# Kernel optimization log

Hardware: AMD Instinct MI355X
Metric: run time of the kernel (lower is better)

## Reference

```python
import jax, jax.numpy as jnp
import numpy as np

N_EXPERTS = 8
D_MODEL = 1024
D_FF = 4096
N_TOKENS = 2048
TOP_K = 2


def _init_expert_weight(key, shape):
    # torch init: bound = sqrt(3) * (sqrt(1/3) / sqrt(fan_in)) = 1/sqrt(fan_in), fan_in = shape[1]
    bound = 1.0 / np.sqrt(shape[1])
    return jax.random.uniform(key, shape, jnp.float32, -bound, bound)


def setup_inputs() -> dict:
    key = jax.random.key(0)
    kx, ki, kw, k1, k2, k3 = jax.random.split(key, 6)
    x = jax.random.normal(kx, (N_TOKENS, D_MODEL), jnp.float32)
    expert_indices = jax.random.randint(ki, (N_TOKENS, TOP_K), 0, N_EXPERTS, jnp.int32)
    expert_weights = jax.random.uniform(kw, (N_TOKENS, TOP_K), jnp.float32)
    w1 = _init_expert_weight(k1, (N_EXPERTS, D_MODEL, D_FF))
    w2 = _init_expert_weight(k2, (N_EXPERTS, D_MODEL, D_FF))
    w3 = _init_expert_weight(k3, (N_EXPERTS, D_FF, D_MODEL))
    return {"x": x, "expert_indices": expert_indices, "expert_weights": expert_weights,
            "w1": w1, "w2": w2, "w3": w3}


def reference(x, expert_indices, expert_weights, w1, w2, w3):
    n_tokens, d_model = x.shape
    top_k = expert_indices.shape[1]
    n_experts = w1.shape[0]
    A = n_tokens * top_k  # total assignments; static capacity per expert (no overflow possible)

    flat_e = expert_indices.reshape(-1)            # [A]
    flat_w = expert_weights.reshape(-1)            # [A]
    tok_idx = jnp.repeat(jnp.arange(n_tokens), top_k)  # [A]

    order = jnp.argsort(flat_e, stable=True)
    s_tok = tok_idx[order]
    s_e = flat_e[order]
    s_w = flat_w[order]

    counts = jnp.bincount(flat_e, length=n_experts)            # [E]
    seg_starts = jnp.concatenate([jnp.zeros((1,), counts.dtype), jnp.cumsum(counts)[:-1]])
    pos = jnp.arange(A) - seg_starts[s_e]                       # position within expert segment

    # dispatch: padded per-expert batch [E, A, d]
    padded = jnp.zeros((n_experts, A, d_model), x.dtype).at[s_e, pos].set(x[s_tok])

    gate = jax.nn.silu(jnp.einsum('ecd,edf->ecf', padded, w1))
    value = jnp.einsum('ecd,edf->ecf', padded, w2)
    hidden = gate * value
    expert_out = jnp.einsum('ecf,efd->ecd', hidden, w3)        # [E, A, d]

    # combine: gather per-assignment outputs, weight, scatter-add back to tokens
    y = expert_out[s_e, pos] * s_w[:, None]                    # [A, d]
    out = jnp.zeros((n_tokens, d_model), x.dtype).at[s_tok].add(y)
    return out
```

## Files before the change

kernel.cpp:

```cpp
#include <hip/hip_runtime.h>
#include <stdint.h>

#define N_EXPERTS 8
#define D_MODEL 1024
#define D_FF 4096
#define N_TOKENS 2048
#define ASSN 4096
#define ROWS 4352
#define BK 64

using bfrag = __attribute__((ext_vector_type(8))) short;
using f32x4 = __attribute__((ext_vector_type(4))) float;
typedef unsigned short u16;

__device__ __forceinline__ u16 f2bf(float f) {
  uint32_t u = __builtin_bit_cast(uint32_t, f);
  u += 0x7fffu + ((u >> 16) & 1u);
  return (u16)(u >> 16);
}

__device__ __forceinline__ void gll16(const void* g, void* l) {
  __builtin_amdgcn_global_load_lds(
      (const __attribute__((address_space(1))) void*)g,
      (__attribute__((address_space(3))) void*)l, 16, 0, 0);
}

__global__ void k_setup(const int* __restrict__ eidx, const float* __restrict__ ew,
                        int* __restrict__ rowmap, int* __restrict__ arow,
                        int* __restrict__ counts, int* __restrict__ offs) {
  __shared__ int sc[N_EXPERTS], so[N_EXPERTS];
  int t = threadIdx.x;
  if (t < N_EXPERTS) sc[t] = 0;
  __syncthreads();
  for (int a = t; a < ASSN; a += 256) atomicAdd(&sc[eidx[a]], 1);
  __syncthreads();
  if (t == 0) {
    int run = 0;
    for (int e = 0; e < N_EXPERTS; e++) {
      counts[e] = sc[e]; offs[e] = run; so[e] = run; run += sc[e];
    }
  }
  __syncthreads();
  for (int a = t; a < ASSN; a += 256) {
    int e = eidx[a];
    int p = atomicAdd(&so[e], 1);
    rowmap[p] = a;
    arow[a] = p;
  }
}

__global__ void k_gather(const float* __restrict__ x, const int* __restrict__ rowmap,
                         u16* __restrict__ Xg) {
  int r = blockIdx.x, t = threadIdx.x;
  uint2 o;
  if (r < ASSN) {
    int tok = rowmap[r] >> 1;
    float4 v = *(const float4*)(x + (size_t)tok * D_MODEL + t * 4);
    o.x = (uint32_t)f2bf(v.x) | ((uint32_t)f2bf(v.y) << 16);
    o.y = (uint32_t)f2bf(v.z) | ((uint32_t)f2bf(v.w) << 16);
  } else {
    o.x = 0u; o.y = 0u;
  }
  *(uint2*)(Xg + (size_t)r * D_MODEL + t * 4) = o;
}

__global__ void k_convt(const float* __restrict__ src, u16* __restrict__ dst,
                        int K, int N) {
  const int e = blockIdx.z;
  src += (size_t)e * K * N;
  dst += (size_t)e * K * N;
  const int n0 = blockIdx.x << 6;
  const int kbase = blockIdx.y << 9;
  __shared__ uint32_t T2[64 * 33];
  const int t = threadIdx.x;
  const int i4 = (t & 15) << 2;
  const int q  = t >> 4;
  const int n = t >> 2, seg = t & 3;
  for (int it = 0; it < 8; ++it) {
    const int k0 = kbase + (it << 6);
    if (it) __syncthreads();
    #pragma unroll
    for (int p = 0; p < 2; p++) {
      const int kp = q + (p << 4);
      const float4 r0 = *(const float4*)(src + (size_t)(k0 + 2 * kp    ) * N + n0 + i4);
      const float4 r1 = *(const float4*)(src + (size_t)(k0 + 2 * kp + 1) * N + n0 + i4);
      T2[(i4 + 0) * 33 + kp] = (uint32_t)f2bf(r0.x) | ((uint32_t)f2bf(r1.x) << 16);
      T2[(i4 + 1) * 33 + kp] = (uint32_t)f2bf(r0.y) | ((uint32_t)f2bf(r1.y) << 16);
      T2[(i4 + 2) * 33 + kp] = (uint32_t)f2bf(r0.z) | ((uint32_t)f2bf(r1.z) << 16);
      T2[(i4 + 3) * 33 + kp] = (uint32_t)f2bf(r0.w) | ((uint32_t)f2bf(r1.w) << 16);
    }
    __syncthreads();
    uint32_t w[8];
    #pragma unroll
    for (int j = 0; j < 8; j++) w[j] = T2[n * 33 + (seg << 3) + j];
    u16* d = dst + (size_t)(n0 + n) * K + k0 + (seg << 4);
    *(uint4*)d = *(uint4*)&w[0];
    *(uint4*)(d + 8) = *(uint4*)&w[4];
  }
}

__launch_bounds__(512, 2)
__global__ void k_gemm1(const u16* __restrict__ Xg,
                        const u16* __restrict__ w1t, const u16* __restrict__ w2t,
                        const int* __restrict__ counts, const int* __restrict__ offs,
                        u16* __restrict__ H) {
  const int e = blockIdx.z, nt = blockIdx.x, mt = blockIdx.y;
  const int cnt = counts[e];
  if (mt * 256 >= cnt) return;
  const int row0 = offs[e] + mt * 256;
  const int mrem = cnt - mt * 256;
  const int n0 = nt * 128;

  __shared__ u16 As[2][256 * BK];
  __shared__ u16 B1s[2][128 * BK];
  __shared__ u16 B2s[2][128 * BK];

  const int tid = threadIdx.x;
  const int lane = tid & 63, wave = tid >> 6;
  const int l16 = lane & 15, quad = lane >> 4;
  const int wm = (wave >> 1) << 6;
  const int wn = (wave & 1) << 6;

  const int swz = ((lane & 7) ^ ((lane >> 3) & 7)) << 3;
  const int arow = wave * 32 + (lane >> 3);
  const int brow = wave * 16 + (lane >> 3);

  const u16* pA  = Xg + (size_t)(row0 + arow) * D_MODEL + swz;
  const size_t ebase = (size_t)e * D_MODEL * D_FF;
  const u16* pB1 = w1t + ebase + (size_t)(n0 + brow) * D_MODEL + swz;
  const u16* pB2 = w2t + ebase + (size_t)(n0 + brow) * D_MODEL + swz;

  const int sA = l16 & 7;
  const int slot0 = ((quad    ) ^ sA) << 3;
  const int slot1 = ((quad + 4) ^ sA) << 3;

  f32x4 acc1[4][4] = {};
  f32x4 acc2[4][4] = {};

#define STAGE1(buf)                                                  \
  do {                                                               \
    gll16(pA,                &As[buf][(wave * 32     ) * BK]);       \
    gll16(pA +  8 * D_MODEL, &As[buf][(wave * 32 +  8) * BK]);       \
    gll16(pA + 16 * D_MODEL, &As[buf][(wave * 32 + 16) * BK]);       \
    gll16(pA + 24 * D_MODEL, &As[buf][(wave * 32 + 24) * BK]);       \
    gll16(pB1,               &B1s[buf][(wave * 16    ) * BK]);       \
    gll16(pB1 + 8 * D_MODEL, &B1s[buf][(wave * 16 + 8) * BK]);       \
    gll16(pB2,               &B2s[buf][(wave * 16    ) * BK]);       \
    gll16(pB2 + 8 * D_MODEL, &B2s[buf][(wave * 16 + 8) * BK]);       \
    pA += BK; pB1 += BK; pB2 += BK;                                  \
  } while (0)

  STAGE1(0);
  for (int t = 0; t < 16; ++t) {
    const int c = t & 1;
    if (t < 15) {
      STAGE1(1 - c);
      asm volatile("s_waitcnt vmcnt(8)" ::: "memory");
    } else {
      asm volatile("s_waitcnt vmcnt(0)" ::: "memory");
    }
    __builtin_amdgcn_sched_barrier(0);
    __builtin_amdgcn_s_barrier();
    __builtin_amdgcn_sched_barrier(0);

    bfrag a0[4], b10[4], b20[4];
    #pragma unroll
    for (int i = 0; i < 4; i++)
      a0[i] = *(const bfrag*)&As[c][(wm + i * 16 + l16) * BK + slot0];
    #pragma unroll
    for (int j = 0; j < 4; j++) {
      b10[j] = *(const bfrag*)&B1s[c][(wn + j * 16 + l16) * BK + slot0];
      b20[j] = *(const bfrag*)&B2s[c][(wn + j * 16 + l16) * BK + slot0];
    }
    asm volatile("s_waitcnt lgkmcnt(0)" ::: "memory");
    __builtin_amdgcn_sched_barrier(0);
    __builtin_amdgcn_s_setprio(1);
    #pragma unroll
    for (int i = 0; i < 4; i++) {
      #pragma unroll
      for (int j = 0; j < 4; j++) {
        acc1[i][j] = __builtin_amdgcn_mfma_f32_16x16x32_bf16(a0[i], b10[j], acc1[i][j], 0, 0, 0);
        acc2[i][j] = __builtin_amdgcn_mfma_f32_16x16x32_bf16(a0[i], b20[j], acc2[i][j], 0, 0, 0);
      }
    }
    __builtin_amdgcn_s_setprio(0);

    bfrag a1[4], b11[4], b21[4];
    #pragma unroll
    for (int i = 0; i < 4; i++)
      a1[i] = *(const bfrag*)&As[c][(wm + i * 16 + l16) * BK + slot1];
    #pragma unroll
    for (int j = 0; j < 4; j++) {
      b11[j] = *(const bfrag*)&B1s[c][(wn + j * 16 + l16) * BK + slot1];
      b21[j] = *(const bfrag*)&B2s[c][(wn + j * 16 + l16) * BK + slot1];
    }
    asm volatile("s_waitcnt lgkmcnt(0)" ::: "memory");
    __builtin_amdgcn_sched_barrier(0);
    __builtin_amdgcn_s_setprio(1);
    #pragma unroll
    for (int i = 0; i < 4; i++) {
      #pragma unroll
      for (int j = 0; j < 4; j++) {
        acc1[i][j] = __builtin_amdgcn_mfma_f32_16x16x32_bf16(a1[i], b11[j], acc1[i][j], 0, 0, 0);
        acc2[i][j] = __builtin_amdgcn_mfma_f32_16x16x32_bf16(a1[i], b21[j], acc2[i][j], 0, 0, 0);
      }
    }
    __builtin_amdgcn_s_setprio(0);

    __builtin_amdgcn_sched_barrier(0);
    __builtin_amdgcn_s_barrier();
    __builtin_amdgcn_sched_barrier(0);
  }
#undef STAGE1

  #pragma unroll
  for (int i = 0; i < 4; i++) {
    #pragma unroll
    for (int p = 0; p < 4; p++) {
      const int mloc = wm + i * 16 + quad * 4 + p;
      if (mloc < mrem) {
        u16* dst = H + (size_t)(row0 + mloc) * D_FF + n0 + wn + l16;
        #pragma unroll
        for (int j = 0; j < 4; j++) {
          float g = acc1[i][j][p];
          float vv = acc2[i][j][p];
          float h = g / (1.0f + __expf(-g)) * vv;
          dst[j * 16] = f2bf(h);
        }
      }
    }
  }
}

__launch_bounds__(512, 2)
__global__ void k_gemm2(const u16* __restrict__ H, const u16* __restrict__ w3t,
                        const int* __restrict__ counts, const int* __restrict__ offs,
                        float* __restrict__ Y0, float* __restrict__ Y1) {
  const int e = blockIdx.z >> 1, khalf = blockIdx.z & 1;
  const int nt = blockIdx.x, mt = blockIdx.y;
  const int cnt = counts[e];
  if (mt * 256 >= cnt) return;
  const int row0 = offs[e] + mt * 256;
  const int mrem = cnt - mt * 256;
  const int n0 = nt * 128;
  float* __restrict__ Y = khalf ? Y1 : Y0;

  __shared__ u16 As[2][256 * BK];
  __shared__ u16 Bs[2][128 * BK];

  const int tid = threadIdx.x;
  const int lane = tid & 63, wave = tid >> 6;
  const int l16 = lane & 15, quad = lane >> 4;
  const int wm = (wave >> 1) << 6;
  const int wn = (wave & 1) << 6;

  const int swz = ((lane & 7) ^ ((lane >> 3) & 7)) << 3;
  const int arow = wave * 32 + (lane >> 3);
  const int brow = wave * 16 + (lane >> 3);

  const u16* pA = H + (size_t)(row0 + arow) * D_FF + khalf * 2048 + swz;
  const u16* pB = w3t + (size_t)e * D_FF * D_MODEL
                + (size_t)(n0 + brow) * D_FF + khalf * 2048 + swz;

  const int sA = l16 & 7;
  const int slot0 = ((quad    ) ^ sA) << 3;
  const int slot1 = ((quad + 4) ^ sA) << 3;

  f32x4 acc[4][4] = {};

#define STAGE2(buf)                                                  \
  do {                                                               \
    gll16(pA,               &As[buf][(wave * 32     ) * BK]);        \
    gll16(pA +  8 * D_FF,   &As[buf][(wave * 32 +  8) * BK]);        \
    gll16(pA + 16 * D_FF,   &As[buf][(wave * 32 + 16) * BK]);        \
    gll16(pA + 24 * D_FF,   &As[buf][(wave * 32 + 24) * BK]);        \
    gll16(pB,               &Bs[buf][(wave * 16    ) * BK]);         \
    gll16(pB + 8 * D_FF,    &Bs[buf][(wave * 16 + 8) * BK]);         \
    pA += BK; pB += BK;                                              \
  } while (0)

  STAGE2(0);
  for (int t = 0; t < 32; ++t) {
    const int c = t & 1;
    if (t < 31) {
      STAGE2(1 - c);
      asm volatile("s_waitcnt vmcnt(6)" ::: "memory");
    } else {
      asm volatile("s_waitcnt vmcnt(0)" ::: "memory");
    }
    __builtin_amdgcn_sched_barrier(0);
    __builtin_amdgcn_s_barrier();
    __builtin_amdgcn_sched_barrier(0);

    bfrag a0[4], b0[4];
    #pragma unroll
    for (int i = 0; i < 4; i++)
      a0[i] = *(const bfrag*)&As[c][(wm + i * 16 + l16) * BK + slot0];
    #pragma unroll
    for (int j = 0; j < 4; j++)
      b0[j] = *(const bfrag*)&Bs[c][(wn + j * 16 + l16) * BK + slot0];
    asm volatile("s_waitcnt lgkmcnt(0)" ::: "memory");
    __builtin_amdgcn_sched_barrier(0);
    __builtin_amdgcn_s_setprio(1);
    #pragma unroll
    for (int i = 0; i < 4; i++) {
      #pragma unroll
      for (int j = 0; j < 4; j++)
        acc[i][j] = __builtin_amdgcn_mfma_f32_16x16x32_bf16(a0[i], b0[j], acc[i][j], 0, 0, 0);
    }
    __builtin_amdgcn_s_setprio(0);

    bfrag a1[4], b1[4];
    #pragma unroll
    for (int i = 0; i < 4; i++)
      a1[i] = *(const bfrag*)&As[c][(wm + i * 16 + l16) * BK + slot1];
    #pragma unroll
    for (int j = 0; j < 4; j++)
      b1[j] = *(const bfrag*)&Bs[c][(wn + j * 16 + l16) * BK + slot1];
    asm volatile("s_waitcnt lgkmcnt(0)" ::: "memory");
    __builtin_amdgcn_sched_barrier(0);
    __builtin_amdgcn_s_setprio(1);
    #pragma unroll
    for (int i = 0; i < 4; i++) {
      #pragma unroll
      for (int j = 0; j < 4; j++)
        acc[i][j] = __builtin_amdgcn_mfma_f32_16x16x32_bf16(a1[i], b1[j], acc[i][j], 0, 0, 0);
    }
    __builtin_amdgcn_s_setprio(0);

    __builtin_amdgcn_sched_barrier(0);
    __builtin_amdgcn_s_barrier();
    __builtin_amdgcn_sched_barrier(0);
  }
#undef STAGE2

  #pragma unroll
  for (int i = 0; i < 4; i++) {
    #pragma unroll
    for (int p = 0; p < 4; p++) {
      const int mloc = wm + i * 16 + quad * 4 + p;
      if (mloc < mrem) {
        float* dst = Y + (size_t)(row0 + mloc) * D_MODEL + n0 + wn + l16;
        #pragma unroll
        for (int j = 0; j < 4; j++) dst[j * 16] = acc[i][j][p];
      }
    }
  }
}

__global__ void k_combine(const float* __restrict__ Y0, const float* __restrict__ Y1,
                          const int* __restrict__ arow, const float* __restrict__ ew,
                          float* __restrict__ out) {
  const int tk = blockIdx.x;
  const int d = threadIdx.x * 4;
  const int a0 = tk * 2, a1 = tk * 2 + 1;
  const int r0 = arow[a0], r1 = arow[a1];
  const float w0 = ew[a0], w1 = ew[a1];
  const float4 p0 = *(const float4*)(Y0 + (size_t)r0 * D_MODEL + d);
  const float4 q0 = *(const float4*)(Y1 + (size_t)r0 * D_MODEL + d);
  const float4 p1 = *(const float4*)(Y0 + (size_t)r1 * D_MODEL + d);
  const float4 q1 = *(const float4*)(Y1 + (size_t)r1 * D_MODEL + d);
  float4 r;
  r.x = w0 * (p0.x + q0.x) + w1 * (p1.x + q1.x);
  r.y = w0 * (p0.y + q0.y) + w1 * (p1.y + q1.y);
  r.z = w0 * (p0.z + q0.z) + w1 * (p1.z + q1.z);
  r.w = w0 * (p0.w + q0.w) + w1 * (p1.w + q1.w);
  *(float4*)(out + (size_t)tk * D_MODEL + d) = r;
}

extern "C" void kernel_launch(void* const* d_in, const int* in_sizes, int n_in,
                              void* d_out, int out_size, void* d_ws, size_t ws_size,
                              hipStream_t stream) {
  const float* x  = (const float*)d_in[0];
  const int* eidx = (const int*)d_in[1];
  const float* ew = (const float*)d_in[2];
  const float* w1 = (const float*)d_in[3];
  const float* w2 = (const float*)d_in[4];
  const float* w3 = (const float*)d_in[5];
  float* out = (float*)d_out;

  char* ws = (char*)d_ws;
  int*   rowmap = (int*)(ws);
  int*   arow   = (int*)(ws + 16384);
  int*   counts = (int*)(ws + 32768);
  int*   offs   = (int*)(ws + 32768 + 64);
  const size_t D0 = 65536;
  const size_t SZ_XG = (size_t)ROWS * D_MODEL * 2;
  const size_t SZ_HB = (size_t)ROWS * D_FF * 2;
  const size_t SZ_Y  = (size_t)ROWS * D_MODEL * 4;
  const size_t SZ_W  = (size_t)N_EXPERTS * D_MODEL * D_FF * 2;
  u16*   Xg  = (u16*)(ws + D0);
  u16*   Hb  = (u16*)(ws + D0 + SZ_XG);
  float* Y0  = (float*)(ws + D0 + SZ_XG + SZ_HB);
  float* Y1  = (float*)(ws + D0 + SZ_XG + SZ_HB + SZ_Y);
  u16*   wt1 = (u16*)(ws + D0 + SZ_XG + SZ_HB + 2 * SZ_Y);
  u16*   wt2 = wt1 + SZ_W / 2;
  u16*   wt3 = wt1;

  k_setup<<<1, 256, 0, stream>>>(eidx, ew, rowmap, arow, counts, offs);
  k_gather<<<ROWS, 256, 0, stream>>>(x, rowmap, Xg);
  k_convt<<<dim3(D_FF / 64, 2, N_EXPERTS), 256, 0, stream>>>(w1, wt1, D_MODEL, D_FF);
  k_convt<<<dim3(D_FF / 64, 2, N_EXPERTS), 256, 0, stream>>>(w2, wt2, D_MODEL, D_FF);
  k_gemm1<<<dim3(D_FF / 128, 16, N_EXPERTS), 512, 0, stream>>>(Xg, wt1, wt2, counts, offs, Hb);
  k_convt<<<dim3(D_MODEL / 64, 8, N_EXPERTS), 256, 0, stream>>>(w3, wt3, D_FF, D_MODEL);
  k_gemm2<<<dim3(D_MODEL / 128, 16, N_EXPERTS * 2), 512, 0, stream>>>(Hb, wt3, counts, offs, Y0, Y1);
  k_combine<<<N_TOKENS, 256, 0, stream>>>(Y0, Y1, arow, ew, out);
}
```

Before: 659.9 us.

## Interleave prefetch with split MFMA phases and flatten weight-transpose grid

The GEMM main loops are restructured into several barrier-separated phases: global-to-LDS prefetches for the next tile are spread across the MFMA phases instead of issued all at once, and B fragments are loaded one matrix at a time to cut register pressure. A full vmcnt(0) wait now sits at the end of each iteration, in place of the partial wait at the start. The weight conversion/transpose kernel is changed so each block handles a single 64x64 tile, giving many more blocks for better occupancy. The extra barriers add synchronization overhead in exchange for finer overlap of loads and compute.

New measurement: 678.5 us. +2.8%, slower.

```diff
diff --git a/kernel.cpp b/kernel.cpp
--- a/kernel.cpp
+++ b/kernel.cpp
@@ -24,6 +24,12 @@
       (const __attribute__((address_space(1))) void*)g,
       (__attribute__((address_space(3))) void*)l, 16, 0, 0);
 }
+
+#define LGKM0_SB()  do { asm volatile("s_waitcnt lgkmcnt(0)" ::: "memory"); \
+                         __builtin_amdgcn_sched_barrier(0); } while (0)
+#define BAR_SB()    do { __builtin_amdgcn_sched_barrier(0); \
+                         __builtin_amdgcn_s_barrier(); \
+                         __builtin_amdgcn_sched_barrier(0); } while (0)
 
 __global__ void k_setup(const int* __restrict__ eidx, const float* __restrict__ ew,
                         int* __restrict__ rowmap, int* __restrict__ arow,
@@ -66,37 +72,34 @@
 
 __global__ void k_convt(const float* __restrict__ src, u16* __restrict__ dst,
                         int K, int N) {
-  const int e = blockIdx.z;
+  const int e = blockIdx.y;
   src += (size_t)e * K * N;
   dst += (size_t)e * K * N;
-  const int n0 = blockIdx.x << 6;
-  const int kbase = blockIdx.y << 9;
+  const int ntn = N >> 6;
+  const int n0 = (blockIdx.x % ntn) << 6;
+  const int k0 = (blockIdx.x / ntn) << 6;
   __shared__ uint32_t T2[64 * 33];
   const int t = threadIdx.x;
   const int i4 = (t & 15) << 2;
   const int q  = t >> 4;
+  #pragma unroll
+  for (int p = 0; p < 2; p++) {
+    const int kp = q + (p << 4);
+    const float4 r0 = *(const float4*)(src + (size_t)(k0 + 2 * kp    ) * N + n0 + i4);
+    const float4 r1 = *(const float4*)(src + (size_t)(k0 + 2 * kp + 1) * N + n0 + i4);
+    T2[(i4 + 0) * 33 + kp] = (uint32_t)f2bf(r0.x) | ((uint32_t)f2bf(r1.x) << 16);
+    T2[(i4 + 1) * 33 + kp] = (uint32_t)f2bf(r0.y) | ((uint32_t)f2bf(r1.y) << 16);
+    T2[(i4 + 2) * 33 + kp] = (uint32_t)f2bf(r0.z) | ((uint32_t)f2bf(r1.z) << 16);
+    T2[(i4 + 3) * 33 + kp] = (uint32_t)f2bf(r0.w) | ((uint32_t)f2bf(r1.w) << 16);
+  }
+  __syncthreads();
   const int n = t >> 2, seg = t & 3;
-  for (int it = 0; it < 8; ++it) {
-    const int k0 = kbase + (it << 6);
-    if (it) __syncthreads();
-    #pragma unroll
-    for (int p = 0; p < 2; p++) {
-      const int kp = q + (p << 4);
-      const float4 r0 = *(const float4*)(src + (size_t)(k0 + 2 * kp    ) * N + n0 + i4);
-      const float4 r1 = *(const float4*)(src + (size_t)(k0 + 2 * kp + 1) * N + n0 + i4);
-      T2[(i4 + 0) * 33 + kp] = (uint32_t)f2bf(r0.x) | ((uint32_t)f2bf(r1.x) << 16);
-      T2[(i4 + 1) * 33 + kp] = (uint32_t)f2bf(r0.y) | ((uint32_t)f2bf(r1.y) << 16);
-      T2[(i4 + 2) * 33 + kp] = (uint32_t)f2bf(r0.z) | ((uint32_t)f2bf(r1.z) << 16);
-      T2[(i4 + 3) * 33 + kp] = (uint32_t)f2bf(r0.w) | ((uint32_t)f2bf(r1.w) << 16);
-    }
-    __syncthreads();
-    uint32_t w[8];
-    #pragma unroll
-    for (int j = 0; j < 8; j++) w[j] = T2[n * 33 + (seg << 3) + j];
-    u16* d = dst + (size_t)(n0 + n) * K + k0 + (seg << 4);
-    *(uint4*)d = *(uint4*)&w[0];
-    *(uint4*)(d + 8) = *(uint4*)&w[4];
-  }
+  uint32_t w[8];
+  #pragma unroll
+  for (int j = 0; j < 8; j++) w[j] = T2[n * 33 + (seg << 3) + j];
+  u16* d = dst + (size_t)(n0 + n) * K + k0 + (seg << 4);
+  *(uint4*)d = *(uint4*)&w[0];
+  *(uint4*)(d + 8) = *(uint4*)&w[4];
 }
 
 __launch_bounds__(512, 2)
@@ -122,13 +125,13 @@
   const int wn = (wave & 1) << 6;
 
   const int swz = ((lane & 7) ^ ((lane >> 3) & 7)) << 3;
-  const int arow = wave * 32 + (lane >> 3);
-  const int brow = wave * 16 + (lane >> 3);
-
-  const u16* pA  = Xg + (size_t)(row0 + arow) * D_MODEL + swz;
+  const int arw = wave * 32 + (lane >> 3);
+  const int brw = wave * 16 + (lane >> 3);
+
+  const u16* pA  = Xg + (size_t)(row0 + arw) * D_MODEL + swz;
   const size_t ebase = (size_t)e * D_MODEL * D_FF;
-  const u16* pB1 = w1t + ebase + (size_t)(n0 + brow) * D_MODEL + swz;
-  const u16* pB2 = w2t + ebase + (size_t)(n0 + brow) * D_MODEL + swz;
+  const u16* pB1 = w1t + ebase + (size_t)(n0 + brw) * D_MODEL + swz;
+  const u16* pB2 = w2t + ebase + (size_t)(n0 + brw) * D_MODEL + swz;
 
   const int sA = l16 & 7;
   const int slot0 = ((quad    ) ^ sA) << 3;
@@ -137,81 +140,103 @@
   f32x4 acc1[4][4] = {};
   f32x4 acc2[4][4] = {};
 
-#define STAGE1(buf)                                                  \
-  do {                                                               \
-    gll16(pA,                &As[buf][(wave * 32     ) * BK]);       \
-    gll16(pA +  8 * D_MODEL, &As[buf][(wave * 32 +  8) * BK]);       \
-    gll16(pA + 16 * D_MODEL, &As[buf][(wave * 32 + 16) * BK]);       \
-    gll16(pA + 24 * D_MODEL, &As[buf][(wave * 32 + 24) * BK]);       \
-    gll16(pB1,               &B1s[buf][(wave * 16    ) * BK]);       \
-    gll16(pB1 + 8 * D_MODEL, &B1s[buf][(wave * 16 + 8) * BK]);       \
-    gll16(pB2,               &B2s[buf][(wave * 16    ) * BK]);       \
-    gll16(pB2 + 8 * D_MODEL, &B2s[buf][(wave * 16 + 8) * BK]);       \
-    pA += BK; pB1 += BK; pB2 += BK;                                  \
-  } while (0)
-
-  STAGE1(0);
+  gll16(pA,                &As[0][(wave * 32     ) * BK]);
+  gll16(pA +  8 * D_MODEL, &As[0][(wave * 32 +  8) * BK]);
+  gll16(pA + 16 * D_MODEL, &As[0][(wave * 32 + 16) * BK]);
+  gll16(pA + 24 * D_MODEL, &As[0][(wave * 32 + 24) * BK]);
+  gll16(pB1,               &B1s[0][(wave * 16    ) * BK]);
+  gll16(pB1 + 8 * D_MODEL, &B1s[0][(wave * 16 + 8) * BK]);
+  gll16(pB2,               &B2s[0][(wave * 16    ) * BK]);
+  gll16(pB2 + 8 * D_MODEL, &B2s[0][(wave * 16 + 8) * BK]);
+  pA += BK; pB1 += BK; pB2 += BK;
+  asm volatile("s_waitcnt vmcnt(0)" ::: "memory");
+  BAR_SB();
+
+  #pragma unroll 2
   for (int t = 0; t < 16; ++t) {
-    const int c = t & 1;
-    if (t < 15) {
-      STAGE1(1 - c);
-      asm volatile("s_waitcnt vmcnt(8)" ::: "memory");
-    } else {
-      asm volatile("s_waitcnt vmcnt(0)" ::: "memory");
-    }
-    __builtin_amdgcn_sched_barrier(0);
-    __builtin_amdgcn_s_barrier();
-    __builtin_amdgcn_sched_barrier(0);
-
-    bfrag a0[4], b10[4], b20[4];
+    const int c = t & 1, nb = 1 - c;
+    const bool pf = (t < 15);
+
+    if (pf) {
+      gll16(pA,               &As[nb][(wave * 32    ) * BK]);
+      gll16(pA + 8 * D_MODEL, &As[nb][(wave * 32 + 8) * BK]);
+    }
+    bfrag a0[4], bt[4];
     #pragma unroll
     for (int i = 0; i < 4; i++)
       a0[i] = *(const bfrag*)&As[c][(wm + i * 16 + l16) * BK + slot0];
     #pragma unroll
-    for (int j = 0; j < 4; j++) {
-      b10[j] = *(const bfrag*)&B1s[c][(wn + j * 16 + l16) * BK + slot0];
-      b20[j] = *(const bfrag*)&B2s[c][(wn + j * 16 + l16) * BK + slot0];
-    }
-    asm volatile("s_waitcnt lgkmcnt(0)" ::: "memory");
-    __builtin_amdgcn_sched_barrier(0);
-    __builtin_amdgcn_s_setprio(1);
-    #pragma unroll
-    for (int i = 0; i < 4; i++) {
-      #pragma unroll
-      for (int j = 0; j < 4; j++) {
-        acc1[i][j] = __builtin_amdgcn_mfma_f32_16x16x32_bf16(a0[i], b10[j], acc1[i][j], 0, 0, 0);
-        acc2[i][j] = __builtin_amdgcn_mfma_f32_16x16x32_bf16(a0[i], b20[j], acc2[i][j], 0, 0, 0);
-      }
-    }
-    __builtin_amdgcn_s_setprio(0);
-
-    bfrag a1[4], b11[4], b21[4];
+    for (int j = 0; j < 4; j++)
+      bt[j] = *(const bfrag*)&B1s[c][(wn + j * 16 + l16) * BK + slot0];
+    BAR_SB();
+    LGKM0_SB();
+    __builtin_amdgcn_s_setprio(1);
+    #pragma unroll
+    for (int i = 0; i < 4; i++)
+      #pragma unroll
+      for (int j = 0; j < 4; j++)
+        acc1[i][j] = __builtin_amdgcn_mfma_f32_16x16x32_bf16(a0[i], bt[j], acc1[i][j], 0, 0, 0);
+    __builtin_amdgcn_s_setprio(0);
+    BAR_SB();
+
+    if (pf) {
+      gll16(pA + 16 * D_MODEL, &As[nb][(wave * 32 + 16) * BK]);
+      gll16(pA + 24 * D_MODEL, &As[nb][(wave * 32 + 24) * BK]);
+    }
+    #pragma unroll
+    for (int j = 0; j < 4; j++)
+      bt[j] = *(const bfrag*)&B2s[c][(wn + j * 16 + l16) * BK + slot0];
+    BAR_SB();
+    LGKM0_SB();
+    __builtin_amdgcn_s_setprio(1);
+    #pragma unroll
+    for (int i = 0; i < 4; i++)
+      #pragma unroll
+      for (int j = 0; j < 4; j++)
+        acc2[i][j] = __builtin_amdgcn_mfma_f32_16x16x32_bf16(a0[i], bt[j], acc2[i][j], 0, 0, 0);
+    __builtin_amdgcn_s_setprio(0);
+    BAR_SB();
+
+    if (pf) {
+      gll16(pB1,               &B1s[nb][(wave * 16    ) * BK]);
+      gll16(pB1 + 8 * D_MODEL, &B1s[nb][(wave * 16 + 8) * BK]);
+      gll16(pB2,               &B2s[nb][(wave * 16    ) * BK]);
+      gll16(pB2 + 8 * D_MODEL, &B2s[nb][(wave * 16 + 8) * BK]);
+      pA += BK; pB1 += BK; pB2 += BK;
+    }
+    bfrag a1[4];
     #pragma unroll
     for (int i = 0; i < 4; i++)
       a1[i] = *(const bfrag*)&As[c][(wm + i * 16 + l16) * BK + slot1];
     #pragma unroll
-    for (int j = 0; j < 4; j++) {
-      b11[j] = *(const bfrag*)&B1s[c][(wn + j * 16 + l16) * BK + slot1];
-      b21[j] = *(const bfrag*)&B2s[c][(wn + j * 16 + l16) * BK + slot1];
-    }
-    asm volatile("s_waitcnt lgkmcnt(0)" ::: "memory");
-    __builtin_amdgcn_sched_barrier(0);
-    __builtin_amdgcn_s_setprio(1);
-    #pragma unroll
-    for (int i = 0; i < 4; i++) {
-      #pragma unroll
-      for (int j = 0; j < 4; j++) {
-        acc1[i][j] = __builtin_amdgcn_mfma_f32_16x16x32_bf16(a1[i], b11[j], acc1[i][j], 0, 0, 0);
-        acc2[i][j] = __builtin_amdgcn_mfma_f32_16x16x32_bf16(a1[i], b21[j], acc2[i][j], 0, 0, 0);
-      }
-    }
-    __builtin_amdgcn_s_setprio(0);
-
-    __builtin_amdgcn_sched_barrier(0);
-    __builtin_amdgcn_s_barrier();
-    __builtin_amdgcn_sched_barrier(0);
-  }
-#undef STAGE1
+    for (int j = 0; j < 4; j++)
+      bt[j] = *(const bfrag*)&B1s[c][(wn + j * 16 + l16) * BK + slot1];
+    BAR_SB();
+    LGKM0_SB();
+    __builtin_amdgcn_s_setprio(1);
+    #pragma unroll
+    for (int i = 0; i < 4; i++)
+      #pragma unroll
+      for (int j = 0; j < 4; j++)
+        acc1[i][j] = __builtin_amdgcn_mfma_f32_16x16x32_bf16(a1[i], bt[j], acc1[i][j], 0, 0, 0);
+    __builtin_amdgcn_s_setprio(0);
+    BAR_SB();
+
+    #pragma unroll
+    for (int j = 0; j < 4; j++)
+      bt[j] = *(const bfrag*)&B2s[c][(wn + j * 16 + l16) * BK + slot1];
+    BAR_SB();
+    LGKM0_SB();
+    __builtin_amdgcn_s_setprio(1);
+    #pragma unroll
+    for (int i = 0; i < 4; i++)
+      #pragma unroll
+      for (int j = 0; j < 4; j++)
+        acc2[i][j] = __builtin_amdgcn_mfma_f32_16x16x32_bf16(a1[i], bt[j], acc2[i][j], 0, 0, 0);
+    __builtin_amdgcn_s_setprio(0);
+    asm volatile("s_waitcnt vmcnt(0)" ::: "memory");
+    BAR_SB();
+  }
 
   #pragma unroll
   for (int i = 0; i < 4; i++) {
@@ -255,12 +280,12 @@
   const int wn = (wave & 1) << 6;
 
   const int swz = ((lane & 7) ^ ((lane >> 3) & 7)) << 3;
-  const int arow = wave * 32 + (lane >> 3);
-  const int brow = wave * 16 + (lane >> 3);
-
-  const u16* pA = H + (size_t)(row0 + arow) * D_FF + khalf * 2048 + swz;
+  const int arw = wave * 32 + (lane >> 3);
+  const int brw = wave * 16 + (lane >> 3);
+
+  const u16* pA = H + (size_t)(row0 + arw) * D_FF + khalf * 2048 + swz;
   const u16* pB = w3t + (size_t)e * D_FF * D_MODEL
-                + (size_t)(n0 + brow) * D_FF + khalf * 2048 + swz;
+                + (size_t)(n0 + brw) * D_FF + khalf * 2048 + swz;
 
   const int sA = l16 & 7;
   const int slot0 = ((quad    ) ^ sA) << 3;
@@ -268,71 +293,67 @@
 
   f32x4 acc[4][4] = {};
 
-#define STAGE2(buf)                                                  \
-  do {                                                               \
-    gll16(pA,               &As[buf][(wave * 32     ) * BK]);        \
-    gll16(pA +  8 * D_FF,   &As[buf][(wave * 32 +  8) * BK]);        \
-    gll16(pA + 16 * D_FF,   &As[buf][(wave * 32 + 16) * BK]);        \
-    gll16(pA + 24 * D_FF,   &As[buf][(wave * 32 + 24) * BK]);        \
-    gll16(pB,               &Bs[buf][(wave * 16    ) * BK]);         \
-    gll16(pB + 8 * D_FF,    &Bs[buf][(wave * 16 + 8) * BK]);         \
-    pA += BK; pB += BK;                                              \
-  } while (0)
-
-  STAGE2(0);
+  gll16(pA,             &As[0][(wave * 32     ) * BK]);
+  gll16(pA +  8 * D_FF, &As[0][(wave * 32 +  8) * BK]);
+  gll16(pA + 16 * D_FF, &As[0][(wave * 32 + 16) * BK]);
+  gll16(pA + 24 * D_FF, &As[0][(wave * 32 + 24) * BK]);
+  gll16(pB,             &Bs[0][(wave * 16    ) * BK]);
+  gll16(pB + 8 * D_FF,  &Bs[0][(wave * 16 + 8) * BK]);
+  pA += BK; pB += BK;
+  asm volatile("s_waitcnt vmcnt(0)" ::: "memory");
+  BAR_SB();
+
+  #pragma unroll 2
   for (int t = 0; t < 32; ++t) {
-    const int c = t & 1;
-    if (t < 31) {
-      STAGE2(1 - c);
-      asm volatile("s_waitcnt vmcnt(6)" ::: "memory");
-    } else {
-      asm volatile("s_waitcnt vmcnt(0)" ::: "memory");
-    }
-    __builtin_amdgcn_sched_barrier(0);
-    __builtin_amdgcn_s_barrier();
-    __builtin_amdgcn_sched_barrier(0);
-
-    bfrag a0[4], b0[4];
+    const int c = t & 1, nb = 1 - c;
+    const bool pf = (t < 31);
+
+    if (pf) {
+      gll16(pA,             &As[nb][(wave * 32     ) * BK]);
+      gll16(pA +  8 * D_FF, &As[nb][(wave * 32 +  8) * BK]);
+      gll16(pA + 16 * D_FF, &As[nb][(wave * 32 + 16) * BK]);
+      gll16(pA + 24 * D_FF, &As[nb][(wave * 32 + 24) * BK]);
+      gll16(pB,             &Bs[nb][(wave * 16    ) * BK]);
+      gll16(pB + 8 * D_FF,  &Bs[nb][(wave * 16 + 8) * BK]);
+      pA += BK; pB += BK;
+    }
+    bfrag a0[4], bt[4];
     #pragma unroll
     for (int i = 0; i < 4; i++)
       a0[i] = *(const bfrag*)&As[c][(wm + i * 16 + l16) * BK + slot0];
     #pragma unroll
     for (int j = 0; j < 4; j++)
-      b0[j] = *(const bfrag*)&Bs[c][(wn + j * 16 + l16) * BK + slot0];
-    asm volatile("s_waitcnt lgkmcnt(0)" ::: "memory");
-    __builtin_amdgcn_sched_barrier(0);
-    __builtin_amdgcn_s_setprio(1);
-    #pragma unroll
-    for (int i = 0; i < 4; i++) {
-      #pragma unroll
-      for (int j = 0; j < 4; j++)
-        acc[i][j] = __builtin_amdgcn_mfma_f32_16x16x32_bf16(a0[i], b0[j], acc[i][j], 0, 0, 0);
-    }
-    __builtin_amdgcn_s_setprio(0);
-
-    bfrag a1[4], b1[4];
+      bt[j] = *(const bfrag*)&Bs[c][(wn + j * 16 + l16) * BK + slot0];
+    BAR_SB();
+    LGKM0_SB();
+    __builtin_amdgcn_s_setprio(1);
+    #pragma unroll
+    for (int i = 0; i < 4; i++)
+      #pragma unroll
+      for (int j = 0; j < 4; j++)
+        acc[i][j] = __builtin_amdgcn_mfma_f32_16x16x32_bf16(a0[i], bt[j], acc[i][j], 0, 0, 0);
+    __builtin_amdgcn_s_setprio(0);
+    BAR_SB();
+
+    bfrag a1[4];
     #pragma unroll
     for (int i = 0; i < 4; i++)
       a1[i] = *(const bfrag*)&As[c][(wm + i * 16 + l16) * BK + slot1];
     #pragma unroll
     for (int j = 0; j < 4; j++)
-      b1[j] = *(const bfrag*)&Bs[c][(wn + j * 16 + l16) * BK + slot1];
-    asm volatile("s_waitcnt lgkmcnt(0)" ::: "memory");
-    __builtin_amdgcn_sched_barrier(0);
-    __builtin_amdgcn_s_setprio(1);
-    #pragma unroll
-    for (int i = 0; i < 4; i++) {
-      #pragma unroll
-      for (int j = 0; j < 4; j++)
-        acc[i][j] = __builtin_amdgcn_mfma_f32_16x16x32_bf16(a1[i], b1[j], acc[i][j], 0, 0, 0);
-    }
-    __builtin_amdgcn_s_setprio(0);
-
-    __builtin_amdgcn_sched_barrier(0);
-    __builtin_amdgcn_s_barrier();
-    __builtin_amdgcn_sched_barrier(0);
-  }
-#undef STAGE2
+      bt[j] = *(const bfrag*)&Bs[c][(wn + j * 16 + l16) * BK + slot1];
+    BAR_SB();
+    LGKM0_SB();
+    __builtin_amdgcn_s_setprio(1);
+    #pragma unroll
+    for (int i = 0; i < 4; i++)
+      #pragma unroll
+      for (int j = 0; j < 4; j++)
+        acc[i][j] = __builtin_amdgcn_mfma_f32_16x16x32_bf16(a1[i], bt[j], acc[i][j], 0, 0, 0);
+    __builtin_amdgcn_s_setprio(0);
+    asm volatile("s_waitcnt vmcnt(0)" ::: "memory");
+    BAR_SB();
+  }
 
   #pragma unroll
   for (int i = 0; i < 4; i++) {
@@ -399,10 +420,10 @@
 
   k_setup<<<1, 256, 0, stream>>>(eidx, ew, rowmap, arow, counts, offs);
   k_gather<<<ROWS, 256, 0, stream>>>(x, rowmap, Xg);
-  k_convt<<<dim3(D_FF / 64, 2, N_EXPERTS), 256, 0, stream>>>(w1, wt1, D_MODEL, D_FF);
-  k_convt<<<dim3(D_FF / 64, 2, N_EXPERTS), 256, 0, stream>>>(w2, wt2, D_MODEL, D_FF);
+  k_convt<<<dim3(1024, N_EXPERTS), 256, 0, stream>>>(w1, wt1, D_MODEL, D_FF);
+  k_convt<<<dim3(1024, N_EXPERTS), 256, 0, stream>>>(w2, wt2, D_MODEL, D_FF);
   k_gemm1<<<dim3(D_FF / 128, 16, N_EXPERTS), 512, 0, stream>>>(Xg, wt1, wt2, counts, offs, Hb);
-  k_convt<<<dim3(D_MODEL / 64, 8, N_EXPERTS), 256, 0, stream>>>(w3, wt3, D_FF, D_MODEL);
+  k_convt<<<dim3(1024, N_EXPERTS), 256, 0, stream>>>(w3, wt3, D_FF, D_MODEL);
   k_gemm2<<<dim3(D_MODEL / 128, 16, N_EXPERTS * 2), 512, 0, stream>>>(Hb, wt3, counts, offs, Y0, Y1);
   k_combine<<<N_TOKENS, 256, 0, stream>>>(Y0, Y1, arow, ew, out);
 }
```
